# Optimization experiments

Measured on AMD Instinct MI355X. Metric: run time of the kernel, lower is better.

## Reference

```python
import jax, jax.numpy as jnp
import numpy as np

N_TOKENS = 8192
D_MODEL = 1024
N_EXPERTS = 8
TOP_K = 2


def setup_inputs() -> dict:
    key = jax.random.key(0)
    ks = jax.random.split(key, 4)
    scale = 1.0 / np.sqrt(D_MODEL)
    x = jax.random.normal(ks[0], (N_TOKENS, D_MODEL), dtype=jnp.float32)
    gate_w = jax.random.uniform(ks[1], (N_EXPERTS, D_MODEL), jnp.float32, -scale, scale)
    expert_w = jax.random.uniform(ks[2], (N_EXPERTS, D_MODEL, D_MODEL), jnp.float32, -scale, scale)
    expert_b = jax.random.uniform(ks[3], (N_EXPERTS, D_MODEL), jnp.float32, -scale, scale)
    return {"x": x, "gate_w": gate_w, "expert_w": expert_w, "expert_b": expert_b}


def reference(x, gate_w, expert_w, expert_b):
    # Router: logits [N, E], softmax in fp32, top-k, renormalize over selected.
    router_logits = jnp.einsum('nd,ed->ne', x, gate_w)
    probs = jax.nn.softmax(router_logits.astype(jnp.float32), axis=1)
    rw, sel = jax.lax.top_k(probs, TOP_K)            # [N, K]
    rw = rw / jnp.sum(rw, axis=-1, keepdims=True)

    # Dense combine weights [N, E]: routing weight for selected experts, 0 else.
    n_idx = jnp.arange(x.shape[0])[:, None]
    w_dense = jnp.zeros((x.shape[0], N_EXPERTS), jnp.float32).at[n_idx, sel].set(rw)

    # Compute all experts for all tokens (vectorized equivalent of the
    # gather -> Linear -> weighted scatter-add loop; zero weight for
    # unselected experts reproduces the sparse dispatch exactly).
    # expert_w[e] is torch nn.Linear weight [out, in]: y = x @ W^T + b
    h = jnp.einsum('nd,ehd->neh', x, expert_w) + expert_b[None, :, :]  # [N, E, H]
    final = jnp.einsum('neh,ne->nh', h, w_dense.astype(x.dtype))
    return final, router_logits
```

## Files before the change

kernel.cpp:

```cpp
#include <hip/hip_runtime.h>
#include <hip/hip_bf16.h>
#include <stdint.h>

#define NT 8192
#define DM 1024
#define NE 8
#define MAX_TILES 160
#define SLOTS_MAX 17408
#define NKT 32

typedef __bf16 bf16x8 __attribute__((ext_vector_type(8)));
typedef float f32x4 __attribute__((ext_vector_type(4)));

typedef const __attribute__((address_space(1))) void* gp_t;
typedef __attribute__((address_space(3))) void* lp_t;
#define GLDS(g, l) __builtin_amdgcn_global_load_lds((gp_t)(g), (lp_t)(l), 16, 0, 0)

__device__ inline unsigned short f2bf(float f) {
  unsigned int u = __float_as_uint(f);
  unsigned int r = (u + 0x7fffu + ((u >> 16) & 1u)) >> 16;
  return (unsigned short)r;
}
__device__ inline float bf2f(unsigned short u) {
  return __uint_as_float((unsigned int)u << 16);
}

__global__ void router_kernel(const float* __restrict__ x,
                              const float* __restrict__ gw,
                              float* __restrict__ logits,
                              unsigned short* __restrict__ xb,
                              int* __restrict__ top2e,
                              float* __restrict__ top2w) {
  const int n = blockIdx.x;
  const int lane = threadIdx.x;
  const float* xr = x + (size_t)n * DM;
  float s[NE];
#pragma unroll
  for (int e = 0; e < NE; ++e) s[e] = 0.f;
  for (int c = lane; c < DM; c += 64) {
    float xv = xr[c];
    xb[(size_t)n * DM + c] = f2bf(xv);
#pragma unroll
    for (int e = 0; e < NE; ++e) s[e] += xv * gw[e * DM + c];
  }
#pragma unroll
  for (int e = 0; e < NE; ++e) {
#pragma unroll
    for (int off = 32; off > 0; off >>= 1) s[e] += __shfl_xor(s[e], off);
  }
  if (lane == 0) {
    float m = s[0];
#pragma unroll
    for (int e = 1; e < NE; ++e) m = fmaxf(m, s[e]);
    float p[NE];
#pragma unroll
    for (int e = 0; e < NE; ++e) {
      p[e] = __expf(s[e] - m);
      logits[(size_t)n * NE + e] = s[e];
    }
    int e1 = 0; float b1 = p[0];
#pragma unroll
    for (int e = 1; e < NE; ++e) if (p[e] > b1) { b1 = p[e]; e1 = e; }
    int e2 = -1; float b2 = -1.f;
#pragma unroll
    for (int e = 0; e < NE; ++e) if (e != e1 && p[e] > b2) { b2 = p[e]; e2 = e; }
    float inv = 1.f / (b1 + b2);
    top2e[n * 2 + 0] = e1; top2e[n * 2 + 1] = e2;
    top2w[n * 2 + 0] = b1 * inv; top2w[n * 2 + 1] = b2 * inv;
  }
}

__global__ void cvt_w_kernel(const float* __restrict__ src,
                             unsigned short* __restrict__ dst) {
  size_t i = ((size_t)blockIdx.x * blockDim.x + threadIdx.x) * 8;
  float4 a = *(const float4*)(src + i);
  float4 b = *(const float4*)(src + i + 4);
  union { unsigned short u[8]; uint4 v; } o;
  o.u[0] = f2bf(a.x); o.u[1] = f2bf(a.y); o.u[2] = f2bf(a.z); o.u[3] = f2bf(a.w);
  o.u[4] = f2bf(b.x); o.u[5] = f2bf(b.y); o.u[6] = f2bf(b.z); o.u[7] = f2bf(b.w);
  *(uint4*)(dst + i) = o.v;
}

__global__ void count_kernel(const int* __restrict__ top2e, int* __restrict__ counts) {
  __shared__ int lcnt[NE];
  const int t = threadIdx.x;
  if (t < NE) lcnt[t] = 0;
  __syncthreads();
  const int n = blockIdx.x * 256 + t;
  atomicAdd(&lcnt[top2e[n * 2 + 0]], 1);
  atomicAdd(&lcnt[top2e[n * 2 + 1]], 1);
  __syncthreads();
  if (t < NE) atomicAdd(&counts[t], lcnt[t]);
}

__global__ void plan_kernel(const int* __restrict__ counts, int* __restrict__ seg_base,
                            int* __restrict__ tile_e, int* __restrict__ tile_row,
                            int* __restrict__ n_tiles) {
  __shared__ int sb[NE + 1], tb[NE + 1];
  const int lane = threadIdx.x;
  if (lane == 0) {
    int base = 0, tt = 0;
    for (int e = 0; e < NE; ++e) {
      sb[e] = base; tb[e] = tt;
      int c = counts[e];
      int nt = (c + 127) >> 7;
      tt += nt;
      base += nt << 7;
    }
    sb[NE] = base; tb[NE] = tt;
    *n_tiles = tt;
  }
  __syncthreads();
  if (lane <= NE) seg_base[lane] = sb[lane];
  const int total = tb[NE];
  for (int i = lane; i < total; i += 64) {
    int e = 0;
#pragma unroll
    for (int q = 0; q < NE; ++q) if (i >= tb[q + 1]) e = q + 1;
    tile_e[i] = e;
    tile_row[i] = sb[e] + (i - tb[e]) * 128;
  }
}

__global__ void scatter_kernel(const int* __restrict__ top2e,
                               const int* __restrict__ seg_base, int* __restrict__ counts2,
                               int* __restrict__ slot_token, int* __restrict__ tok2slot) {
  __shared__ int lcnt[NE], lbase[NE];
  const int t = threadIdx.x;
  if (t < NE) lcnt[t] = 0;
  __syncthreads();
  const int n = blockIdx.x * 256 + t;
  const int e0 = top2e[n * 2 + 0], e1 = top2e[n * 2 + 1];
  const int p0 = atomicAdd(&lcnt[e0], 1);
  const int p1 = atomicAdd(&lcnt[e1], 1);
  __syncthreads();
  if (t < NE) lbase[t] = seg_base[t] + atomicAdd(&counts2[t], lcnt[t]);
  __syncthreads();
  const int q0 = lbase[e0] + p0, q1 = lbase[e1] + p1;
  slot_token[q0] = n; slot_token[q1] = n;
  tok2slot[n * 2 + 0] = q0;
  tok2slot[n * 2 + 1] = q1;
}

__global__ __launch_bounds__(256, 4) void moe_gemm_kernel(
    const unsigned short* __restrict__ xb,
    const unsigned short* __restrict__ wb,
    const float* __restrict__ bias,
    const int* __restrict__ slot_token,
    const int* __restrict__ tile_e, const int* __restrict__ tile_row,
    const int* __restrict__ n_tiles,
    unsigned short* __restrict__ y)
{
  const int bid = blockIdx.x;
  const int swz = (bid & 7) * 160 + (bid >> 3);
  const int bm = swz >> 3;
  const int bn = swz & 7;
  if (bm >= *n_tiles) return;
  const int e = tile_e[bm];
  const int row0 = tile_row[bm];
  const int n0 = bn * 128;

  __shared__ __align__(16) unsigned short lA[2][4096];
  __shared__ __align__(16) unsigned short lB[2][4096];

  const int t = threadIdx.x;
  const int lane = t & 63;
  const int w = t >> 6;
  const int wm = w >> 1, wn = w & 1;

  const int sS = (t & 7) ^ ((t >> 3) & 7);
  const unsigned short* asrc[2];
  const unsigned short* bsrc[2];
#pragma unroll
  for (int c = 0; c < 2; ++c) {
    const int lr = c * 64 + ((t >> 3) << 1) + (sS >> 2);
    const int tok = slot_token[row0 + lr];
    asrc[c] = xb + (size_t)tok * DM + (sS & 3) * 8;
    bsrc[c] = wb + (size_t)e * DM * DM + (size_t)(n0 + lr) * DM + (sS & 3) * 8;
  }

  f32x4 acc[4][4];
#pragma unroll
  for (int i = 0; i < 4; ++i)
#pragma unroll
    for (int j = 0; j < 4; ++j) acc[i][j] = (f32x4){0.f, 0.f, 0.f, 0.f};

  auto stage = [&](int buf, int kt) {
    const int ko = kt * 32;
#pragma unroll
    for (int c = 0; c < 2; ++c) {
      GLDS(asrc[c] + ko, &lA[buf][c * 2048 + t * 8]);
      GLDS(bsrc[c] + ko, &lB[buf][c * 2048 + t * 8]);
    }
  };

  stage(0, 0);
  stage(1, 1);

  const int q = lane >> 4;
  for (int kt = 0; kt < NKT; ++kt) {
    if (kt < NKT - 1) {
      asm volatile("s_waitcnt vmcnt(4)" ::: "memory");
    } else {
      asm volatile("s_waitcnt vmcnt(0)" ::: "memory");
    }
    __builtin_amdgcn_sched_barrier(0);
    __builtin_amdgcn_s_barrier();

    const int cur = kt & 1;
    bf16x8 af[4], bf[4];
#pragma unroll
    for (int mi = 0; mi < 4; ++mi) {
      const int row = wm * 64 + mi * 16 + (lane & 15);
      const int off = (row >> 1) * 128 + (((((row & 1) << 2) | q) ^ ((row >> 1) & 7)) << 4);
      af[mi] = *(const bf16x8*)((const char*)lA[cur] + off);
    }
#pragma unroll
    for (int ni = 0; ni < 4; ++ni) {
      const int row = wn * 64 + ni * 16 + (lane & 15);
      const int off = (row >> 1) * 128 + (((((row & 1) << 2) | q) ^ ((row >> 1) & 7)) << 4);
      bf[ni] = *(const bf16x8*)((const char*)lB[cur] + off);
    }
    __builtin_amdgcn_s_setprio(1);
#pragma unroll
    for (int mi = 0; mi < 4; ++mi)
#pragma unroll
      for (int ni = 0; ni < 4; ++ni)
        acc[mi][ni] = __builtin_amdgcn_mfma_f32_16x16x32_bf16(af[mi], bf[ni], acc[mi][ni], 0, 0, 0);
    __builtin_amdgcn_s_setprio(0);

    __builtin_amdgcn_sched_barrier(0);
    __builtin_amdgcn_s_barrier();
    if (kt + 2 < NKT) stage(cur, kt + 2);
  }

  const int cgrp = lane >> 4, ccol = lane & 15;
  float bv[4];
#pragma unroll
  for (int ni = 0; ni < 4; ++ni)
    bv[ni] = bias[e * DM + n0 + wn * 64 + ni * 16 + ccol];
#pragma unroll
  for (int mi = 0; mi < 4; ++mi) {
#pragma unroll
    for (int j = 0; j < 4; ++j) {
      const int r = row0 + wm * 64 + mi * 16 + cgrp * 4 + j;
      unsigned short* yrow = y + (size_t)r * DM + n0 + wn * 64;
#pragma unroll
      for (int ni = 0; ni < 4; ++ni)
        yrow[ni * 16 + ccol] = f2bf(acc[mi][ni][j] + bv[ni]);
    }
  }
}

__global__ void combine_kernel(const unsigned short* __restrict__ y,
                               const int* __restrict__ tok2slot,
                               const float* __restrict__ top2w,
                               float* __restrict__ out) {
  const int n = blockIdx.x;
  const int c = threadIdx.x;
  const int s0 = tok2slot[n * 2 + 0], s1 = tok2slot[n * 2 + 1];
  const float w0 = top2w[n * 2 + 0], w1 = top2w[n * 2 + 1];
  ushort4 a = *(const ushort4*)(y + (size_t)s0 * DM + c * 4);
  ushort4 b = *(const ushort4*)(y + (size_t)s1 * DM + c * 4);
  float4 r;
  r.x = w0 * bf2f(a.x) + w1 * bf2f(b.x);
  r.y = w0 * bf2f(a.y) + w1 * bf2f(b.y);
  r.z = w0 * bf2f(a.z) + w1 * bf2f(b.z);
  r.w = w0 * bf2f(a.w) + w1 * bf2f(b.w);
  *(float4*)(out + (size_t)n * DM + c * 4) = r;
}

extern "C" void kernel_launch(void* const* d_in, const int* in_sizes, int n_in,
                              void* d_out, int out_size, void* d_ws, size_t ws_size,
                              hipStream_t stream) {
  const float* x  = (const float*)d_in[0];
  const float* gw = (const float*)d_in[1];
  const float* ew = (const float*)d_in[2];
  const float* eb = (const float*)d_in[3];
  float* out    = (float*)d_out;
  float* logits = out + (size_t)NT * DM;

  char* ws = (char*)d_ws;
  int*   counts     = (int*)(ws + 0);
  int*   counts2    = (int*)(ws + 64);
  int*   seg_base   = (int*)(ws + 128);
  int*   n_tiles    = (int*)(ws + 192);
  int*   tile_e     = (int*)(ws + 256);
  int*   tile_row   = (int*)(ws + 1024);
  int*   top2e      = (int*)(ws + 2048);
  float* top2w      = (float*)(ws + 67584);
  int*   slot_token = (int*)(ws + 133120);
  int*   tok2slot   = (int*)(ws + 202752);
  unsigned short* xb = (unsigned short*)(ws + 272384);
  unsigned short* wb = (unsigned short*)(ws + 272384 + 16777216);
  unsigned short* y  = (unsigned short*)(ws + 272384 + 2 * 16777216);

  hipMemsetAsync(ws, 0, 256, stream);
  hipMemsetAsync(slot_token, 0, (size_t)SLOTS_MAX * 4, stream);

  cvt_w_kernel<<<(NE * DM * DM) / 8 / 256, 256, 0, stream>>>(ew, wb);
  router_kernel<<<NT, 64, 0, stream>>>(x, gw, logits, xb, top2e, top2w);
  count_kernel<<<NT / 256, 256, 0, stream>>>(top2e, counts);
  plan_kernel<<<1, 64, 0, stream>>>(counts, seg_base, tile_e, tile_row, n_tiles);
  scatter_kernel<<<NT / 256, 256, 0, stream>>>(top2e, seg_base, counts2, slot_token, tok2slot);
  moe_gemm_kernel<<<MAX_TILES * 8, 256, 0, stream>>>(xb, wb, eb, slot_token,
                                                     tile_e, tile_row, n_tiles, y);
  combine_kernel<<<NT, 256, 0, stream>>>(y, tok2slot, top2w, out);
}
```

Baseline: 112.0 us.

## Load expert weight fragments directly to registers instead of staging through LDS

The B operand (expert weights) is now loaded straight from global memory into per-wave register fragments with a two-deep register double buffer, and only the gathered token tile A still goes through LDS. This halves LDS footprint and LDS read traffic, and drops the B swizzle. In exchange each wave issues its own global loads for B, so the two waves sharing a column block no longer share one fetch and global/L2 traffic for weights doubles. Register pressure also rises, so launch bounds drop occupancy from 4 to 3 blocks per CU.

```diff
diff --git a/kernel.cpp b/kernel.cpp
--- a/kernel.cpp
+++ b/kernel.cpp
@@ -142,7 +142,7 @@
   tok2slot[n * 2 + 1] = q1;
 }
 
-__global__ __launch_bounds__(256, 4) void moe_gemm_kernel(
+__global__ __launch_bounds__(256, 3) void moe_gemm_kernel(
     const unsigned short* __restrict__ xb,
     const unsigned short* __restrict__ wb,
     const float* __restrict__ bias,
@@ -161,7 +161,6 @@
   const int n0 = bn * 128;
 
   __shared__ __align__(16) unsigned short lA[2][4096];
-  __shared__ __align__(16) unsigned short lB[2][4096];
 
   const int t = threadIdx.x;
   const int lane = t & 63;
@@ -170,14 +169,18 @@
 
   const int sS = (t & 7) ^ ((t >> 3) & 7);
   const unsigned short* asrc[2];
-  const unsigned short* bsrc[2];
 #pragma unroll
   for (int c = 0; c < 2; ++c) {
     const int lr = c * 64 + ((t >> 3) << 1) + (sS >> 2);
     const int tok = slot_token[row0 + lr];
     asrc[c] = xb + (size_t)tok * DM + (sS & 3) * 8;
-    bsrc[c] = wb + (size_t)e * DM * DM + (size_t)(n0 + lr) * DM + (sS & 3) * 8;
-  }
+  }
+
+  const unsigned short* bptr[4];
+#pragma unroll
+  for (int ni = 0; ni < 4; ++ni)
+    bptr[ni] = wb + (size_t)e * DM * DM
+             + (size_t)(n0 + wn * 64 + ni * 16 + (lane & 15)) * DM + (lane >> 4) * 8;
 
   f32x4 acc[4][4];
 #pragma unroll
@@ -185,53 +188,54 @@
 #pragma unroll
     for (int j = 0; j < 4; ++j) acc[i][j] = (f32x4){0.f, 0.f, 0.f, 0.f};
 
-  auto stage = [&](int buf, int kt) {
+  auto stageA = [&](int buf, int kt) {
     const int ko = kt * 32;
-#pragma unroll
-    for (int c = 0; c < 2; ++c) {
-      GLDS(asrc[c] + ko, &lA[buf][c * 2048 + t * 8]);
-      GLDS(bsrc[c] + ko, &lB[buf][c * 2048 + t * 8]);
-    }
+    GLDS(asrc[0] + ko, &lA[buf][t * 8]);
+    GLDS(asrc[1] + ko, &lA[buf][2048 + t * 8]);
   };
-
-  stage(0, 0);
-  stage(1, 1);
+  auto loadB = [&](bf16x8* bq, int kt) {
+#pragma unroll
+    for (int ni = 0; ni < 4; ++ni)
+      bq[ni] = *(const bf16x8*)(bptr[ni] + kt * 32);
+  };
+
+  bf16x8 bqA[4], bqB[4];
+  stageA(0, 0); loadB(bqA, 0);
+  stageA(1, 1); loadB(bqB, 1);
 
   const int q = lane >> 4;
-  for (int kt = 0; kt < NKT; ++kt) {
-    if (kt < NKT - 1) {
-      asm volatile("s_waitcnt vmcnt(4)" ::: "memory");
+  auto body = [&](int kt, bf16x8* bq, int buf) {
+    if (kt + 1 < NKT) {
+      asm volatile("s_waitcnt vmcnt(6)" ::: "memory");
     } else {
       asm volatile("s_waitcnt vmcnt(0)" ::: "memory");
     }
     __builtin_amdgcn_sched_barrier(0);
     __builtin_amdgcn_s_barrier();
 
-    const int cur = kt & 1;
-    bf16x8 af[4], bf[4];
+    bf16x8 af[4];
 #pragma unroll
     for (int mi = 0; mi < 4; ++mi) {
       const int row = wm * 64 + mi * 16 + (lane & 15);
       const int off = (row >> 1) * 128 + (((((row & 1) << 2) | q) ^ ((row >> 1) & 7)) << 4);
-      af[mi] = *(const bf16x8*)((const char*)lA[cur] + off);
-    }
-#pragma unroll
-    for (int ni = 0; ni < 4; ++ni) {
-      const int row = wn * 64 + ni * 16 + (lane & 15);
-      const int off = (row >> 1) * 128 + (((((row & 1) << 2) | q) ^ ((row >> 1) & 7)) << 4);
-      bf[ni] = *(const bf16x8*)((const char*)lB[cur] + off);
+      af[mi] = *(const bf16x8*)((const char*)lA[buf] + off);
     }
     __builtin_amdgcn_s_setprio(1);
 #pragma unroll
     for (int mi = 0; mi < 4; ++mi)
 #pragma unroll
       for (int ni = 0; ni < 4; ++ni)
-        acc[mi][ni] = __builtin_amdgcn_mfma_f32_16x16x32_bf16(af[mi], bf[ni], acc[mi][ni], 0, 0, 0);
+        acc[mi][ni] = __builtin_amdgcn_mfma_f32_16x16x32_bf16(af[mi], bq[ni], acc[mi][ni], 0, 0, 0);
     __builtin_amdgcn_s_setprio(0);
 
     __builtin_amdgcn_sched_barrier(0);
     __builtin_amdgcn_s_barrier();
-    if (kt + 2 < NKT) stage(cur, kt + 2);
+    if (kt + 2 < NKT) { stageA(buf, kt + 2); loadB(bq, kt + 2); }
+  };
+
+  for (int kt = 0; kt < NKT; kt += 2) {
+    body(kt, bqA, 0);
+    body(kt + 1, bqB, 1);
   }
 
   const int cgrp = lane >> 4, ccol = lane & 15;
```

Result: slower. 144.7 us (+29.2%).

## Triple-buffer MoE GEMM LDS pipeline and fuse expert counting into router

Applied to the files above, without the earlier changes.

The expert GEMM moves from double to triple LDS buffering. Prefetch of tile k+2 is issued right after the barrier, which removes the second per-iteration barrier, and the A-fragment LDS reads are split into two halves interleaved with the MFMAs. The router now processes four tokens per block and accumulates per-expert counts in shared memory, eliminating the separate count kernel launch. The cost is more LDS per block and fewer guaranteed resident blocks (launch bound 4 to 3).

```diff
diff --git a/kernel.cpp b/kernel.cpp
--- a/kernel.cpp
+++ b/kernel.cpp
@@ -30,9 +30,14 @@
                               float* __restrict__ logits,
                               unsigned short* __restrict__ xb,
                               int* __restrict__ top2e,
-                              float* __restrict__ top2w) {
-  const int n = blockIdx.x;
-  const int lane = threadIdx.x;
+                              float* __restrict__ top2w,
+                              int* __restrict__ counts) {
+  __shared__ int lcnt[NE];
+  const int t = threadIdx.x;
+  if (t < NE) lcnt[t] = 0;
+  __syncthreads();
+  const int lane = t & 63;
+  const int n = blockIdx.x * 4 + (t >> 6);
   const float* xr = x + (size_t)n * DM;
   float s[NE];
 #pragma unroll
@@ -67,7 +72,11 @@
     float inv = 1.f / (b1 + b2);
     top2e[n * 2 + 0] = e1; top2e[n * 2 + 1] = e2;
     top2w[n * 2 + 0] = b1 * inv; top2w[n * 2 + 1] = b2 * inv;
-  }
+    atomicAdd(&lcnt[e1], 1);
+    atomicAdd(&lcnt[e2], 1);
+  }
+  __syncthreads();
+  if (t < NE) atomicAdd(&counts[t], lcnt[t]);
 }
 
 __global__ void cvt_w_kernel(const float* __restrict__ src,
@@ -79,18 +88,6 @@
   o.u[0] = f2bf(a.x); o.u[1] = f2bf(a.y); o.u[2] = f2bf(a.z); o.u[3] = f2bf(a.w);
   o.u[4] = f2bf(b.x); o.u[5] = f2bf(b.y); o.u[6] = f2bf(b.z); o.u[7] = f2bf(b.w);
   *(uint4*)(dst + i) = o.v;
-}
-
-__global__ void count_kernel(const int* __restrict__ top2e, int* __restrict__ counts) {
-  __shared__ int lcnt[NE];
-  const int t = threadIdx.x;
-  if (t < NE) lcnt[t] = 0;
-  __syncthreads();
-  const int n = blockIdx.x * 256 + t;
-  atomicAdd(&lcnt[top2e[n * 2 + 0]], 1);
-  atomicAdd(&lcnt[top2e[n * 2 + 1]], 1);
-  __syncthreads();
-  if (t < NE) atomicAdd(&counts[t], lcnt[t]);
 }
 
 __global__ void plan_kernel(const int* __restrict__ counts, int* __restrict__ seg_base,
@@ -142,7 +139,7 @@
   tok2slot[n * 2 + 1] = q1;
 }
 
-__global__ __launch_bounds__(256, 4) void moe_gemm_kernel(
+__global__ __launch_bounds__(256, 3) void moe_gemm_kernel(
     const unsigned short* __restrict__ xb,
     const unsigned short* __restrict__ wb,
     const float* __restrict__ bias,
@@ -160,8 +157,8 @@
   const int row0 = tile_row[bm];
   const int n0 = bn * 128;
 
-  __shared__ __align__(16) unsigned short lA[2][4096];
-  __shared__ __align__(16) unsigned short lB[2][4096];
+  __shared__ __align__(16) unsigned short lA[3][4096];
+  __shared__ __align__(16) unsigned short lB[3][4096];
 
   const int t = threadIdx.x;
   const int lane = t & 63;
@@ -198,6 +195,8 @@
   stage(1, 1);
 
   const int q = lane >> 4;
+  const int l15 = lane & 15;
+  int cur = 0;
   for (int kt = 0; kt < NKT; ++kt) {
     if (kt < NKT - 1) {
       asm volatile("s_waitcnt vmcnt(4)" ::: "memory");
@@ -206,32 +205,47 @@
     }
     __builtin_amdgcn_sched_barrier(0);
     __builtin_amdgcn_s_barrier();
-
-    const int cur = kt & 1;
-    bf16x8 af[4], bf[4];
-#pragma unroll
-    for (int mi = 0; mi < 4; ++mi) {
-      const int row = wm * 64 + mi * 16 + (lane & 15);
-      const int off = (row >> 1) * 128 + (((((row & 1) << 2) | q) ^ ((row >> 1) & 7)) << 4);
-      af[mi] = *(const bf16x8*)((const char*)lA[cur] + off);
-    }
+    __builtin_amdgcn_sched_barrier(0);
+
+    int nxt = cur + 2; if (nxt >= 3) nxt -= 3;
+    if (kt + 2 < NKT) stage(nxt, kt + 2);
+
+    bf16x8 bf[4], af0, af1, af2, af3;
 #pragma unroll
     for (int ni = 0; ni < 4; ++ni) {
-      const int row = wn * 64 + ni * 16 + (lane & 15);
+      const int row = wn * 64 + ni * 16 + l15;
       const int off = (row >> 1) * 128 + (((((row & 1) << 2) | q) ^ ((row >> 1) & 7)) << 4);
       bf[ni] = *(const bf16x8*)((const char*)lB[cur] + off);
     }
+    {
+      const int r0 = wm * 64 + l15;
+      af0 = *(const bf16x8*)((const char*)lA[cur] + (r0 >> 1) * 128 + (((((r0 & 1) << 2) | q) ^ ((r0 >> 1) & 7)) << 4));
+      const int r1 = wm * 64 + 16 + l15;
+      af1 = *(const bf16x8*)((const char*)lA[cur] + (r1 >> 1) * 128 + (((((r1 & 1) << 2) | q) ^ ((r1 >> 1) & 7)) << 4));
+    }
     __builtin_amdgcn_s_setprio(1);
 #pragma unroll
-    for (int mi = 0; mi < 4; ++mi)
-#pragma unroll
-      for (int ni = 0; ni < 4; ++ni)
-        acc[mi][ni] = __builtin_amdgcn_mfma_f32_16x16x32_bf16(af[mi], bf[ni], acc[mi][ni], 0, 0, 0);
+    for (int ni = 0; ni < 4; ++ni) {
+      acc[0][ni] = __builtin_amdgcn_mfma_f32_16x16x32_bf16(af0, bf[ni], acc[0][ni], 0, 0, 0);
+      acc[1][ni] = __builtin_amdgcn_mfma_f32_16x16x32_bf16(af1, bf[ni], acc[1][ni], 0, 0, 0);
+    }
     __builtin_amdgcn_s_setprio(0);
 
-    __builtin_amdgcn_sched_barrier(0);
-    __builtin_amdgcn_s_barrier();
-    if (kt + 2 < NKT) stage(cur, kt + 2);
+    {
+      const int r2 = wm * 64 + 32 + l15;
+      af2 = *(const bf16x8*)((const char*)lA[cur] + (r2 >> 1) * 128 + (((((r2 & 1) << 2) | q) ^ ((r2 >> 1) & 7)) << 4));
+      const int r3 = wm * 64 + 48 + l15;
+      af3 = *(const bf16x8*)((const char*)lA[cur] + (r3 >> 1) * 128 + (((((r3 & 1) << 2) | q) ^ ((r3 >> 1) & 7)) << 4));
+    }
+    __builtin_amdgcn_s_setprio(1);
+#pragma unroll
+    for (int ni = 0; ni < 4; ++ni) {
+      acc[2][ni] = __builtin_amdgcn_mfma_f32_16x16x32_bf16(af2, bf[ni], acc[2][ni], 0, 0, 0);
+      acc[3][ni] = __builtin_amdgcn_mfma_f32_16x16x32_bf16(af3, bf[ni], acc[3][ni], 0, 0, 0);
+    }
+    __builtin_amdgcn_s_setprio(0);
+
+    cur = (cur == 2) ? 0 : cur + 1;
   }
 
   const int cgrp = lane >> 4, ccol = lane & 15;
@@ -299,8 +313,7 @@
   hipMemsetAsync(slot_token, 0, (size_t)SLOTS_MAX * 4, stream);
 
   cvt_w_kernel<<<(NE * DM * DM) / 8 / 256, 256, 0, stream>>>(ew, wb);
-  router_kernel<<<NT, 64, 0, stream>>>(x, gw, logits, xb, top2e, top2w);
-  count_kernel<<<NT / 256, 256, 0, stream>>>(top2e, counts);
+  router_kernel<<<NT / 4, 256, 0, stream>>>(x, gw, logits, xb, top2e, top2w, counts);
   plan_kernel<<<1, 64, 0, stream>>>(counts, seg_base, tile_e, tile_row, n_tiles);
   scatter_kernel<<<NT / 256, 256, 0, stream>>>(top2e, seg_base, counts2, slot_token, tok2slot);
   moe_gemm_kernel<<<MAX_TILES * 8, 256, 0, stream>>>(xb, wb, eb, slot_token,
```

New measurement: 127.5 us. +13.9%, slower.
